# Kernel tuning notes

Measured on AMD Instinct MI355X. Metric: run time of the kernel, lower is better.

## Reference

```python
import jax, jax.numpy as jnp
import numpy as np

EMBD_DIM = 768
NUM_HEADS = 12
DEPTH = EMBD_DIM // NUM_HEADS


def setup_inputs() -> dict:
    key = jax.random.key(0)
    ks = jax.random.split(key, 8)
    B, S, D = 4, 2048, EMBD_DIM
    scale = 1.0 / np.sqrt(D)
    return {
        "q": jax.random.normal(ks[0], (B, S, D), dtype=jnp.float32),
        "k": jax.random.normal(ks[1], (B, S, D), dtype=jnp.float32),
        "v": jax.random.normal(ks[2], (B, S, D), dtype=jnp.float32),
        # torch nn.Linear stores weight as [out, in]; y = x @ W.T
        "wq": jax.random.normal(ks[3], (D, D), dtype=jnp.float32) * scale,
        "wk": jax.random.normal(ks[4], (D, D), dtype=jnp.float32) * scale,
        "wv": jax.random.normal(ks[5], (D, D), dtype=jnp.float32) * scale,
        "wd": jax.random.normal(ks[6], (D, D), dtype=jnp.float32) * scale,
        "bd": jax.random.normal(ks[7], (D,), dtype=jnp.float32) * 0.01,
    }


def _split_heads(x):
    B, S, _ = x.shape
    return x.reshape(B, S, NUM_HEADS, DEPTH).transpose(0, 2, 1, 3)  # [B,H,S,depth]


def reference(q, k, v, wq, wk, wv, wd, bd):
    B, S, D = q.shape
    qh = _split_heads(q @ wq.T)
    kh = _split_heads(k @ wk.T)
    vh = _split_heads(v @ wv.T)
    scale = jnp.sqrt(jnp.float32(DEPTH))
    logits = jnp.einsum("bhqd,bhkd->bhqk", qh, kh) / scale  # [B,H,S,S]
    attn = jax.nn.softmax(logits, axis=-1)
    ctx = jnp.einsum("bhqk,bhkd->bhqd", attn, vh)
    ctx = ctx.transpose(0, 2, 1, 3).reshape(B, S, D)
    out = ctx @ wd.T + bd
    return out, attn[:, 0, :, :]
```

## Files before the change

### kernel.cpp

```cpp
#include <hip/hip_runtime.h>
#include <stdint.h>

typedef unsigned short u16;
typedef __attribute__((ext_vector_type(8))) __bf16 bf16x8;
typedef __attribute__((ext_vector_type(4))) float f32x4;

#define BSD 6291456
#define WSZ 589824

__device__ __forceinline__ u16 f2bf(float f) {
  union { float f; uint32_t u; } v; v.f = f;
  return (u16)((v.u + 0x7fff + ((v.u >> 16) & 1)) >> 16);
}

__device__ __forceinline__ void load_lds16(const u16* g, u16* l) {
  __builtin_amdgcn_global_load_lds((__attribute__((address_space(1))) void*)(void*)g,
                                   (__attribute__((address_space(3))) void*)l, 16, 0, 0);
}

__device__ __forceinline__ f32x4 mfma16(bf16x8 a, bf16x8 b, f32x4 c) {
  return __builtin_amdgcn_mfma_f32_16x16x32_bf16(a, b, c, 0, 0, 0);
}

__global__ void convert_all(const float* __restrict__ q, const float* __restrict__ k,
                            const float* __restrict__ v, const float* __restrict__ wq,
                            const float* __restrict__ wk, const float* __restrict__ wv,
                            const float* __restrict__ wd, u16* __restrict__ ws) {
  long e = ((long)blockIdx.x * blockDim.x + threadIdx.x) * 8;
  const float* src;
  if (e < (long)BSD) src = q + e;
  else if (e < 2L*BSD) src = k + (e - (long)BSD);
  else if (e < 3L*BSD) src = v + (e - 2L*BSD);
  else {
    long r = e - 3L*BSD;
    if (r < (long)WSZ) src = wq + r;
    else if (r < 2L*WSZ) src = wk + (r - (long)WSZ);
    else if (r < 3L*WSZ) src = wv + (r - 2L*WSZ);
    else src = wd + (r - 3L*WSZ);
  }
  float4 f0 = ((const float4*)src)[0];
  float4 f1 = ((const float4*)src)[1];
  union { u16 s[8]; uint4 u; } o;
  o.s[0]=f2bf(f0.x); o.s[1]=f2bf(f0.y); o.s[2]=f2bf(f0.z); o.s[3]=f2bf(f0.w);
  o.s[4]=f2bf(f1.x); o.s[5]=f2bf(f1.y); o.s[6]=f2bf(f1.z); o.s[7]=f2bf(f1.w);
  *(uint4*)(ws + e) = o.u;
}

template<int OUTF32>
__global__ __launch_bounds__(256) void gemm_bt(const u16* __restrict__ A, const u16* __restrict__ Bm,
                                               u16* __restrict__ Cb, float* __restrict__ Cf,
                                               const float* __restrict__ bias, int M, int N, int K) {
  __shared__ u16 ldsA[128*32];
  __shared__ u16 ldsB[128*32];
  const int t = threadIdx.x, w = t >> 6, lane = t & 63, quad = lane >> 4, n16 = lane & 15;
  const int m0 = blockIdx.x * 128, n0 = blockIdx.y * 128;
  const int wr = (w >> 1) * 64, wc = (w & 1) * 64;
  f32x4 acc[4][4] = {};
  for (int k0 = 0; k0 < K; k0 += 32) {
    __syncthreads();
#pragma unroll
    for (int j = 0; j < 2; ++j) {
      int slot = j*256 + w*64 + lane;
      int row = slot >> 2, ch = slot & 3;
      load_lds16(A  + (size_t)(m0 + row)*K + k0 + ch*8, ldsA + slot*8);
      load_lds16(Bm + (size_t)(n0 + row)*K + k0 + ch*8, ldsB + slot*8);
    }
    __syncthreads();
    bf16x8 af[4], bf[4];
#pragma unroll
    for (int i = 0; i < 4; ++i) {
      af[i] = *(const bf16x8*)(ldsA + (wr + i*16 + n16)*32 + quad*8);
      bf[i] = *(const bf16x8*)(ldsB + (wc + i*16 + n16)*32 + quad*8);
    }
#pragma unroll
    for (int mi = 0; mi < 4; ++mi)
#pragma unroll
      for (int ni = 0; ni < 4; ++ni)
        acc[mi][ni] = mfma16(af[mi], bf[ni], acc[mi][ni]);
  }
#pragma unroll
  for (int mi = 0; mi < 4; ++mi)
#pragma unroll
    for (int ni = 0; ni < 4; ++ni)
#pragma unroll
      for (int i = 0; i < 4; ++i) {
        size_t r = (size_t)m0 + wr + mi*16 + quad*4 + i;
        size_t c = (size_t)n0 + wc + ni*16 + n16;
        float val = acc[mi][ni][i];
        if (OUTF32) Cf[r*(size_t)N + c] = val + bias[c];
        else        Cb[r*(size_t)N + c] = f2bf(val);
      }
}

__global__ __launch_bounds__(256) void transpose_v(const u16* __restrict__ Vh, u16* __restrict__ Vt) {
  __shared__ u16 tile[64][72];
  const int b = blockIdx.z, h = blockIdx.y, st = blockIdx.x;
  const int t = threadIdx.x;
#pragma unroll
  for (int i = 0; i < 16; ++i) {
    int e = i*256 + t;
    int s = e >> 6, d = e & 63;
    tile[s][d] = Vh[(size_t)(b*2048 + st*64 + s)*768 + h*64 + d];
  }
  __syncthreads();
#pragma unroll
  for (int i = 0; i < 16; ++i) {
    int e = i*256 + t;
    int d = e >> 6, s = e & 63;
    Vt[((size_t)(b*12 + h)*64 + d)*2048 + st*64 + s] = tile[s][d];
  }
}

__global__ __launch_bounds__(256, 4) void attn_fused(const u16* __restrict__ Qh, const u16* __restrict__ Kh,
                                                     const u16* __restrict__ Vt, u16* __restrict__ ctx,
                                                     float* __restrict__ rowsum) {
  __shared__ u16 ldsK[64*64];
  __shared__ u16 ldsV[64*64];
  __shared__ u16 ldsP[128*64];
  const int qt = blockIdx.x, h = blockIdx.y, b = blockIdx.z;
  const int t = threadIdx.x, w = t >> 6, lane = t & 63, quad = lane >> 4, n16 = lane & 15;
  const int q0 = qt * 128;
  const int sw = n16 & 7;
  const u16* Kbh = Kh + (size_t)b*2048*768 + h*64;
  const u16* Vbh = Vt + (size_t)(b*12 + h)*64*2048;
  bf16x8 qf[2][2];
#pragma unroll
  for (int mi = 0; mi < 2; ++mi)
#pragma unroll
    for (int ks = 0; ks < 2; ++ks)
      qf[mi][ks] = *(const bf16x8*)(Qh + (size_t)(b*2048 + q0 + w*32 + mi*16 + n16)*768
                                       + h*64 + ks*32 + quad*8);
  f32x4 oacc[2][4] = {};
  float rs[2] = {};
  const float escale = 0.18033688f;
#pragma unroll 1
  for (int c = 0; c < 32; ++c) {
    __syncthreads();
#pragma unroll
    for (int j = 0; j < 2; ++j) {
      int slot = j*256 + t;
      int n = slot >> 3, cg = (slot & 7) ^ (n & 7);
      load_lds16(Kbh + (size_t)(c*64 + n)*768 + cg*8, ldsK + slot*8);
      load_lds16(Vbh + (size_t)n*2048 + c*64 + cg*8, ldsV + slot*8);
    }
    __syncthreads();
    f32x4 sacc[4][2] = {};
#pragma unroll
    for (int ni = 0; ni < 4; ++ni) {
      const u16* krow = ldsK + (ni*16 + n16)*64;
      bf16x8 kf0 = *(const bf16x8*)(krow + ((0 + quad) ^ sw)*8);
      bf16x8 kf1 = *(const bf16x8*)(krow + ((4 + quad) ^ sw)*8);
#pragma unroll
      for (int mi = 0; mi < 2; ++mi) {
        sacc[ni][mi] = mfma16(kf0, qf[mi][0], sacc[ni][mi]);
        sacc[ni][mi] = mfma16(kf1, qf[mi][1], sacc[ni][mi]);
      }
    }
#pragma unroll
    for (int mi = 0; mi < 2; ++mi) {
      int m = w*32 + mi*16 + n16;
      u16* prow = ldsP + m*64 + (quad & 1)*4;
#pragma unroll
      for (int ni = 0; ni < 4; ++ni) {
        float p0 = exp2f(sacc[ni][mi][0] * escale);
        float p1 = exp2f(sacc[ni][mi][1] * escale);
        float p2 = exp2f(sacc[ni][mi][2] * escale);
        float p3 = exp2f(sacc[ni][mi][3] * escale);
        rs[mi] += (p0 + p1) + (p2 + p3);
        uint2 pk;
        pk.x = (uint32_t)f2bf(p0) | ((uint32_t)f2bf(p1) << 16);
        pk.y = (uint32_t)f2bf(p2) | ((uint32_t)f2bf(p3) << 16);
        int c128 = ((ni*2 + (quad >> 1)) ^ sw);
        *(uint2*)(prow + c128*8) = pk;
      }
    }
#pragma unroll
    for (int kt = 0; kt < 2; ++kt) {
      bf16x8 pf[2], vf[4];
#pragma unroll
      for (int mi = 0; mi < 2; ++mi)
        pf[mi] = *(const bf16x8*)(ldsP + (w*32 + mi*16 + n16)*64 + ((kt*4 + quad) ^ sw)*8);
#pragma unroll
      for (int di = 0; di < 4; ++di)
        vf[di] = *(const bf16x8*)(ldsV + (di*16 + n16)*64 + ((kt*4 + quad) ^ sw)*8);
#pragma unroll
      for (int mi = 0; mi < 2; ++mi)
#pragma unroll
        for (int di = 0; di < 4; ++di)
          oacc[mi][di] = mfma16(pf[mi], vf[di], oacc[mi][di]);
    }
  }
#pragma unroll
  for (int mi = 0; mi < 2; ++mi) {
    float s = rs[mi];
    s += __shfl_xor(s, 16);
    s += __shfl_xor(s, 32);
    rs[mi] = s;
  }
  float invr[2][4];
#pragma unroll
  for (int mi = 0; mi < 2; ++mi)
#pragma unroll
    for (int i = 0; i < 4; ++i)
      invr[mi][i] = 1.0f / __shfl(rs[mi], (lane & 48) | (quad*4 + i));
#pragma unroll
  for (int mi = 0; mi < 2; ++mi)
#pragma unroll
    for (int di = 0; di < 4; ++di)
#pragma unroll
      for (int i = 0; i < 4; ++i) {
        size_t r = (size_t)b*2048 + q0 + w*32 + mi*16 + quad*4 + i;
        int cc = h*64 + di*16 + n16;
        ctx[r*768 + cc] = f2bf(oacc[mi][di][i] * invr[mi][i]);
      }
  if (h == 0 && quad == 0) {
#pragma unroll
    for (int mi = 0; mi < 2; ++mi)
      rowsum[b*2048 + q0 + w*32 + mi*16 + n16] = rs[mi];
  }
}

__global__ __launch_bounds__(256) void attn_h0(const u16* __restrict__ Qh, const u16* __restrict__ Kh,
                                               const float* __restrict__ rowsum, float* __restrict__ aout) {
  __shared__ u16 ldsK[128*64];
  const int qt = blockIdx.x, kt = blockIdx.y, b = blockIdx.z;
  const int t = threadIdx.x, w = t >> 6, lane = t & 63, quad = lane >> 4, n16 = lane & 15;
  const int q0 = qt * 128;
  const u16* Kbh = Kh + (size_t)b*2048*768;
  bf16x8 qf[2][2];
#pragma unroll
  for (int mi = 0; mi < 2; ++mi)
#pragma unroll
    for (int ks = 0; ks < 2; ++ks)
      qf[mi][ks] = *(const bf16x8*)(Qh + (size_t)(b*2048 + q0 + w*32 + mi*16 + n16)*768
                                       + ks*32 + quad*8);
#pragma unroll
  for (int j = 0; j < 4; ++j) {
    int slot = j*256 + w*64 + lane;
    int n = slot >> 3, cs = slot & 7, cg = cs ^ (n & 7);
    load_lds16(Kbh + (size_t)(kt*128 + n)*768 + cg*8, ldsK + slot*8);
  }
  __syncthreads();
  f32x4 sacc[2][8] = {};
#pragma unroll
  for (int ni = 0; ni < 8; ++ni) {
    int n = ni*16 + n16;
    bf16x8 kf0 = *(const bf16x8*)(ldsK + n*64 + ((quad)     ^ (n & 7))*8);
    bf16x8 kf1 = *(const bf16x8*)(ldsK + n*64 + ((4 + quad) ^ (n & 7))*8);
#pragma unroll
    for (int mi = 0; mi < 2; ++mi) {
      sacc[mi][ni] = mfma16(qf[mi][0], kf0, sacc[mi][ni]);
      sacc[mi][ni] = mfma16(qf[mi][1], kf1, sacc[mi][ni]);
    }
  }
  float inv[2][4];
#pragma unroll
  for (int mi = 0; mi < 2; ++mi)
#pragma unroll
    for (int i = 0; i < 4; ++i)
      inv[mi][i] = 1.0f / rowsum[b*2048 + q0 + w*32 + mi*16 + quad*4 + i];
#pragma unroll
  for (int mi = 0; mi < 2; ++mi)
#pragma unroll
    for (int ni = 0; ni < 8; ++ni)
#pragma unroll
      for (int i = 0; i < 4; ++i) {
        size_t r = (size_t)b*2048 + q0 + w*32 + mi*16 + quad*4 + i;
        size_t cc = (size_t)kt*128 + ni*16 + n16;
        aout[r*2048 + cc] = __expf(sacc[mi][ni][i] * 0.125f) * inv[mi][i];
      }
}

extern "C" void kernel_launch(void* const* d_in, const int* in_sizes, int n_in,
                              void* d_out, int out_size, void* d_ws, size_t ws_size,
                              hipStream_t stream) {
  (void)in_sizes; (void)n_in; (void)out_size; (void)ws_size;
  const float* q  = (const float*)d_in[0];
  const float* k  = (const float*)d_in[1];
  const float* v  = (const float*)d_in[2];
  const float* wq = (const float*)d_in[3];
  const float* wk = (const float*)d_in[4];
  const float* wv = (const float*)d_in[5];
  const float* wd = (const float*)d_in[6];
  const float* bd = (const float*)d_in[7];

  u16* ws  = (u16*)d_ws;
  u16* qb  = ws;
  u16* kb  = ws + (size_t)BSD;
  u16* vb  = ws + 2L*BSD;
  u16* wqb = ws + 3L*BSD;
  u16* wkb = wqb + WSZ;
  u16* wvb = wqb + 2L*WSZ;
  u16* wdb = wqb + 3L*WSZ;
  u16* Qh  = ws + 3L*BSD + 4L*WSZ;
  u16* Kh  = Qh + (size_t)BSD;
  float* rsum = (float*)(Kh + (size_t)BSD);
  u16* Vh  = kb;
  u16* Vt  = qb;
  u16* ctx = vb;
  float* out  = (float*)d_out;
  float* aout = out + (size_t)BSD;

  convert_all<<<dim3(10368), 256, 0, stream>>>(q, k, v, wq, wk, wv, wd, ws);
  dim3 gp(64, 6);
  gemm_bt<0><<<gp, 256, 0, stream>>>(qb, wqb, Qh, nullptr, nullptr, 8192, 768, 768);
  gemm_bt<0><<<gp, 256, 0, stream>>>(kb, wkb, Kh, nullptr, nullptr, 8192, 768, 768);
  gemm_bt<0><<<gp, 256, 0, stream>>>(vb, wvb, Vh, nullptr, nullptr, 8192, 768, 768);
  transpose_v<<<dim3(32, 12, 4), 256, 0, stream>>>(Vh, Vt);
  attn_fused<<<dim3(16, 12, 4), 256, 0, stream>>>(Qh, Kh, Vt, ctx, rsum);
  attn_h0<<<dim3(16, 16, 4), 256, 0, stream>>>(Qh, Kh, rsum, aout);
  gemm_bt<1><<<gp, 256, 0, stream>>>(ctx, wdb, nullptr, out, bd, 8192, 768, 768);
}
```

Measured before the change: 366.0 us.

## Fuse QK projections, fold softmax scale into Q, transpose V in GEMM epilogue, double-buffer attention

Merges the Q and K projection GEMMs into a single launch and writes V directly in transposed per-head layout from the GEMM epilogue, removing the separate transpose kernel. The softmax scale (including log2e) is folded into Q so attention uses a raw hardware exp2. K/V tiles in the attention kernel are double-buffered to overlap loads with MFMA work, with occupancy hint lowered to 3. bf16 packing uses a perm-based rounding instead of bitwise per-element conversion. Risks include the hidden dependence on contiguous workspace layout and the approximate rounding (no ties-to-even) in packing.

```diff
diff --git a/kernel.cpp b/kernel.cpp
--- a/kernel.cpp
+++ b/kernel.cpp
@@ -7,10 +7,23 @@
 
 #define BSD 6291456
 #define WSZ 589824
-
+#define QSCALE 0.18033688011112042f
+
+#if __has_builtin(__builtin_amdgcn_exp2f)
+#define EXP2(x) __builtin_amdgcn_exp2f(x)
+#else
+#define EXP2(x) __builtin_exp2f(x)
+#endif
+
+__device__ __forceinline__ uint32_t fbits(float f) {
+  union { float f; uint32_t u; } v; v.f = f; return v.u;
+}
 __device__ __forceinline__ u16 f2bf(float f) {
-  union { float f; uint32_t u; } v; v.f = f;
-  return (u16)((v.u + 0x7fff + ((v.u >> 16) & 1)) >> 16);
+  uint32_t u = fbits(f);
+  return (u16)((u + 0x7fff + ((u >> 16) & 1)) >> 16);
+}
+__device__ __forceinline__ uint32_t pack_bf16rn(float lo, float hi) {
+  return __builtin_amdgcn_perm(fbits(hi) + 0x8000u, fbits(lo) + 0x8000u, 0x07060302u);
 }
 
 __device__ __forceinline__ void load_lds16(const u16* g, u16* l) {
@@ -40,21 +53,27 @@
   }
   float4 f0 = ((const float4*)src)[0];
   float4 f1 = ((const float4*)src)[1];
-  union { u16 s[8]; uint4 u; } o;
-  o.s[0]=f2bf(f0.x); o.s[1]=f2bf(f0.y); o.s[2]=f2bf(f0.z); o.s[3]=f2bf(f0.w);
-  o.s[4]=f2bf(f1.x); o.s[5]=f2bf(f1.y); o.s[6]=f2bf(f1.z); o.s[7]=f2bf(f1.w);
-  *(uint4*)(ws + e) = o.u;
-}
-
-template<int OUTF32>
-__global__ __launch_bounds__(256) void gemm_bt(const u16* __restrict__ A, const u16* __restrict__ Bm,
+  uint4 o;
+  o.x = pack_bf16rn(f0.x, f0.y);
+  o.y = pack_bf16rn(f0.z, f0.w);
+  o.z = pack_bf16rn(f1.x, f1.y);
+  o.w = pack_bf16rn(f1.z, f1.w);
+  *(uint4*)(ws + e) = o;
+}
+
+template<int MODE, int BSEL>
+__global__ __launch_bounds__(256) void gemm_bt(const u16* __restrict__ A, const u16* __restrict__ Bw,
                                                u16* __restrict__ Cb, float* __restrict__ Cf,
-                                               const float* __restrict__ bias, int M, int N, int K) {
+                                               const float* __restrict__ bias,
+                                               int M, int N, int K, float oscale) {
   __shared__ u16 ldsA[128*32];
   __shared__ u16 ldsB[128*32];
   const int t = threadIdx.x, w = t >> 6, lane = t & 63, quad = lane >> 4, n16 = lane & 15;
   const int m0 = blockIdx.x * 128, n0 = blockIdx.y * 128;
   const int wr = (w >> 1) * 64, wc = (w & 1) * 64;
+  const u16* Bm = Bw;
+  float sc = oscale;
+  if (BSEL && m0 >= 8192) { Bm = Bw + WSZ; sc = 1.0f; }
   f32x4 acc[4][4] = {};
   for (int k0 = 0; k0 < K; k0 += 32) {
     __syncthreads();
@@ -81,41 +100,34 @@
 #pragma unroll
   for (int mi = 0; mi < 4; ++mi)
 #pragma unroll
-    for (int ni = 0; ni < 4; ++ni)
-#pragma unroll
-      for (int i = 0; i < 4; ++i) {
-        size_t r = (size_t)m0 + wr + mi*16 + quad*4 + i;
-        size_t c = (size_t)n0 + wc + ni*16 + n16;
-        float val = acc[mi][ni][i];
-        if (OUTF32) Cf[r*(size_t)N + c] = val + bias[c];
-        else        Cb[r*(size_t)N + c] = f2bf(val);
-      }
-}
-
-__global__ __launch_bounds__(256) void transpose_v(const u16* __restrict__ Vh, u16* __restrict__ Vt) {
-  __shared__ u16 tile[64][72];
-  const int b = blockIdx.z, h = blockIdx.y, st = blockIdx.x;
-  const int t = threadIdx.x;
-#pragma unroll
-  for (int i = 0; i < 16; ++i) {
-    int e = i*256 + t;
-    int s = e >> 6, d = e & 63;
-    tile[s][d] = Vh[(size_t)(b*2048 + st*64 + s)*768 + h*64 + d];
-  }
-  __syncthreads();
-#pragma unroll
-  for (int i = 0; i < 16; ++i) {
-    int e = i*256 + t;
-    int d = e >> 6, s = e & 63;
-    Vt[((size_t)(b*12 + h)*64 + d)*2048 + st*64 + s] = tile[s][d];
-  }
-}
-
-__global__ __launch_bounds__(256, 4) void attn_fused(const u16* __restrict__ Qh, const u16* __restrict__ Kh,
+    for (int ni = 0; ni < 4; ++ni) {
+      if (MODE == 2) {
+        int c = n0 + wc + ni*16 + n16;
+        int hh = c >> 6, d = c & 63;
+        int m = m0 + wr + mi*16 + quad*4;
+        int bI = m >> 11, s = m & 2047;
+        uint2 pk;
+        pk.x = pack_bf16rn(acc[mi][ni][0], acc[mi][ni][1]);
+        pk.y = pack_bf16rn(acc[mi][ni][2], acc[mi][ni][3]);
+        *(uint2*)(Cb + ((size_t)(bI*12 + hh)*64 + d)*2048 + s) = pk;
+      } else {
+#pragma unroll
+        for (int i = 0; i < 4; ++i) {
+          size_t r = (size_t)m0 + wr + mi*16 + quad*4 + i;
+          size_t c = (size_t)n0 + wc + ni*16 + n16;
+          float val = acc[mi][ni][i];
+          if (MODE == 1) Cf[r*(size_t)N + c] = val + bias[c];
+          else           Cb[r*(size_t)N + c] = f2bf(val * sc);
+        }
+      }
+    }
+}
+
+__global__ __launch_bounds__(256, 3) void attn_fused(const u16* __restrict__ Qh, const u16* __restrict__ Kh,
                                                      const u16* __restrict__ Vt, u16* __restrict__ ctx,
                                                      float* __restrict__ rowsum) {
-  __shared__ u16 ldsK[64*64];
-  __shared__ u16 ldsV[64*64];
+  __shared__ u16 ldsK[2][64*64];
+  __shared__ u16 ldsV[2][64*64];
   __shared__ u16 ldsP[128*64];
   const int qt = blockIdx.x, h = blockIdx.y, b = blockIdx.z;
   const int t = threadIdx.x, w = t >> 6, lane = t & 63, quad = lane >> 4, n16 = lane & 15;
@@ -123,6 +135,15 @@
   const int sw = n16 & 7;
   const u16* Kbh = Kh + (size_t)b*2048*768 + h*64;
   const u16* Vbh = Vt + (size_t)(b*12 + h)*64*2048;
+  auto stage = [&](int c, int bsel) {
+#pragma unroll
+    for (int j = 0; j < 2; ++j) {
+      int slot = j*256 + t;
+      int n = slot >> 3, cg = (slot & 7) ^ (n & 7);
+      load_lds16(Kbh + (size_t)(c*64 + n)*768 + cg*8, &ldsK[bsel][0] + slot*8);
+      load_lds16(Vbh + (size_t)n*2048 + c*64 + cg*8, &ldsV[bsel][0] + slot*8);
+    }
+  };
   bf16x8 qf[2][2];
 #pragma unroll
   for (int mi = 0; mi < 2; ++mi)
@@ -132,22 +153,17 @@
                                        + h*64 + ks*32 + quad*8);
   f32x4 oacc[2][4] = {};
   float rs[2] = {};
-  const float escale = 0.18033688f;
+  stage(0, 0);
 #pragma unroll 1
   for (int c = 0; c < 32; ++c) {
     __syncthreads();
-#pragma unroll
-    for (int j = 0; j < 2; ++j) {
-      int slot = j*256 + t;
-      int n = slot >> 3, cg = (slot & 7) ^ (n & 7);
-      load_lds16(Kbh + (size_t)(c*64 + n)*768 + cg*8, ldsK + slot*8);
-      load_lds16(Vbh + (size_t)n*2048 + c*64 + cg*8, ldsV + slot*8);
-    }
-    __syncthreads();
+    if (c < 31) stage(c + 1, (c + 1) & 1);
+    const u16* K0 = &ldsK[c & 1][0];
+    const u16* V0 = &ldsV[c & 1][0];
     f32x4 sacc[4][2] = {};
 #pragma unroll
     for (int ni = 0; ni < 4; ++ni) {
-      const u16* krow = ldsK + (ni*16 + n16)*64;
+      const u16* krow = K0 + (ni*16 + n16)*64;
       bf16x8 kf0 = *(const bf16x8*)(krow + ((0 + quad) ^ sw)*8);
       bf16x8 kf1 = *(const bf16x8*)(krow + ((4 + quad) ^ sw)*8);
 #pragma unroll
@@ -162,14 +178,14 @@
       u16* prow = ldsP + m*64 + (quad & 1)*4;
 #pragma unroll
       for (int ni = 0; ni < 4; ++ni) {
-        float p0 = exp2f(sacc[ni][mi][0] * escale);
-        float p1 = exp2f(sacc[ni][mi][1] * escale);
-        float p2 = exp2f(sacc[ni][mi][2] * escale);
-        float p3 = exp2f(sacc[ni][mi][3] * escale);
+        float p0 = EXP2(sacc[ni][mi][0]);
+        float p1 = EXP2(sacc[ni][mi][1]);
+        float p2 = EXP2(sacc[ni][mi][2]);
+        float p3 = EXP2(sacc[ni][mi][3]);
         rs[mi] += (p0 + p1) + (p2 + p3);
         uint2 pk;
-        pk.x = (uint32_t)f2bf(p0) | ((uint32_t)f2bf(p1) << 16);
-        pk.y = (uint32_t)f2bf(p2) | ((uint32_t)f2bf(p3) << 16);
+        pk.x = pack_bf16rn(p0, p1);
+        pk.y = pack_bf16rn(p2, p3);
         int c128 = ((ni*2 + (quad >> 1)) ^ sw);
         *(uint2*)(prow + c128*8) = pk;
       }
@@ -182,7 +198,7 @@
         pf[mi] = *(const bf16x8*)(ldsP + (w*32 + mi*16 + n16)*64 + ((kt*4 + quad) ^ sw)*8);
 #pragma unroll
       for (int di = 0; di < 4; ++di)
-        vf[di] = *(const bf16x8*)(ldsV + (di*16 + n16)*64 + ((kt*4 + quad) ^ sw)*8);
+        vf[di] = *(const bf16x8*)(V0 + (di*16 + n16)*64 + ((kt*4 + quad) ^ sw)*8);
 #pragma unroll
       for (int mi = 0; mi < 2; ++mi)
 #pragma unroll
@@ -267,7 +283,7 @@
       for (int i = 0; i < 4; ++i) {
         size_t r = (size_t)b*2048 + q0 + w*32 + mi*16 + quad*4 + i;
         size_t cc = (size_t)kt*128 + ni*16 + n16;
-        aout[r*2048 + cc] = __expf(sacc[mi][ni][i] * 0.125f) * inv[mi][i];
+        aout[r*2048 + cc] = EXP2(sacc[mi][ni][i]) * inv[mi][i];
       }
 }
 
@@ -289,25 +305,20 @@
   u16* kb  = ws + (size_t)BSD;
   u16* vb  = ws + 2L*BSD;
   u16* wqb = ws + 3L*BSD;
-  u16* wkb = wqb + WSZ;
   u16* wvb = wqb + 2L*WSZ;
   u16* wdb = wqb + 3L*WSZ;
   u16* Qh  = ws + 3L*BSD + 4L*WSZ;
   u16* Kh  = Qh + (size_t)BSD;
   float* rsum = (float*)(Kh + (size_t)BSD);
-  u16* Vh  = kb;
   u16* Vt  = qb;
-  u16* ctx = vb;
+  u16* ctx = kb;
   float* out  = (float*)d_out;
   float* aout = out + (size_t)BSD;
 
   convert_all<<<dim3(10368), 256, 0, stream>>>(q, k, v, wq, wk, wv, wd, ws);
-  dim3 gp(64, 6);
-  gemm_bt<0><<<gp, 256, 0, stream>>>(qb, wqb, Qh, nullptr, nullptr, 8192, 768, 768);
-  gemm_bt<0><<<gp, 256, 0, stream>>>(kb, wkb, Kh, nullptr, nullptr, 8192, 768, 768);
-  gemm_bt<0><<<gp, 256, 0, stream>>>(vb, wvb, Vh, nullptr, nullptr, 8192, 768, 768);
-  transpose_v<<<dim3(32, 12, 4), 256, 0, stream>>>(Vh, Vt);
+  gemm_bt<0,1><<<dim3(128, 6), 256, 0, stream>>>(qb, wqb, Qh, nullptr, nullptr, 16384, 768, 768, QSCALE);
+  gemm_bt<2,0><<<dim3(64, 6), 256, 0, stream>>>(vb, wvb, Vt, nullptr, nullptr, 8192, 768, 768, 1.0f);
   attn_fused<<<dim3(16, 12, 4), 256, 0, stream>>>(Qh, Kh, Vt, ctx, rsum);
   attn_h0<<<dim3(16, 16, 4), 256, 0, stream>>>(Qh, Kh, rsum, aout);
-  gemm_bt<1><<<gp, 256, 0, stream>>>(ctx, wdb, nullptr, out, bd, 8192, 768, 768);
-}
+  gemm_bt<1,0><<<dim3(64, 6), 256, 0, stream>>>(ctx, wdb, nullptr, out, bd, 8192, 768, 768, 1.0f);
+}
```

New measurement: 322.9 us. 11.8% less time.
